# Kernel tuning notes

Hardware: AMD Instinct MI355X
Metric: run time of the kernel (lower is better)

The kernel has to match this reference:

```python
import jax, jax.numpy as jnp
import numpy as np

N = 20000
E = 600000
D = 512
H = 8
HD = D // H
HID = 1024
FIN = D + 3 * H  # forces_mlp input dim = 536
SCALE = 1.0 / float(np.sqrt(HD))


def _ln(x, g, b, eps=1e-5):
    m = x.mean(-1, keepdims=True)
    v = x.var(-1, keepdims=True)
    return (x - m) / jnp.sqrt(v + eps) * g + b


def _resmlp(h, Wi, bi, Wh, bh, Wo, bo):
    # ResMLP with layers=3: in-proj, one residual hidden block, out-proj
    h = jax.nn.gelu(h @ Wi + bi)
    h = h + jax.nn.gelu(h @ Wh + bh)
    return h @ Wo + bo


def setup_inputs() -> dict:
    key = jax.random.key(0)
    ks = jax.random.split(key, 24)
    s = 0.02
    x = jax.random.normal(ks[0], (N, D), jnp.float32)
    edge_index = jax.random.randint(ks[1], (2, E), 0, N, dtype=jnp.int32)
    att_bias = jax.random.normal(ks[2], (E,), jnp.float32)
    pos = jax.random.normal(ks[3], (N, 3), jnp.float32)
    batch = jnp.zeros((N,), jnp.int32)
    return {
        "x": x, "edge_index": edge_index, "att_bias": att_bias, "pos": pos, "batch": batch,
        "g_att": jnp.ones((D,), jnp.float32), "b_att": jnp.zeros((D,), jnp.float32),
        "g_mlp": jnp.ones((D,), jnp.float32), "b_mlp": jnp.zeros((D,), jnp.float32),
        "Wq": jax.random.normal(ks[4], (D, D), jnp.float32) * s, "bq": jnp.zeros((D,), jnp.float32),
        "Wk": jax.random.normal(ks[5], (D, D), jnp.float32) * s, "bk": jnp.zeros((D,), jnp.float32),
        "We_in": jax.random.normal(ks[6], (D, HID), jnp.float32) * s, "be_in": jnp.zeros((HID,), jnp.float32),
        "We_h": jax.random.normal(ks[7], (HID, HID), jnp.float32) * s, "be_h": jnp.zeros((HID,), jnp.float32),
        "We_out": jax.random.normal(ks[8], (HID, 1), jnp.float32) * s, "be_out": jnp.zeros((1,), jnp.float32),
        "Wf_in": jax.random.normal(ks[9], (FIN, HID), jnp.float32) * s, "bf_in": jnp.zeros((HID,), jnp.float32),
        "Wf_h": jax.random.normal(ks[10], (HID, HID), jnp.float32) * s, "bf_h": jnp.zeros((HID,), jnp.float32),
        "Wf_out": jax.random.normal(ks[11], (HID, 3), jnp.float32) * s, "bf_out": jnp.zeros((3,), jnp.float32),
    }


def reference(x, edge_index, att_bias, pos, batch,
              g_att, b_att, g_mlp, b_mlp, Wq, bq, Wk, bk,
              We_in, be_in, We_h, be_h, We_out, be_out,
              Wf_in, bf_in, Wf_h, bf_h, Wf_out, bf_out):
    n = x.shape[0]
    row, col = edge_index[0], edge_index[1]

    z_att = _ln(x, g_att, b_att)
    q = (z_att @ Wq + bq).reshape(n, H, HD)  # [N,H,HD]
    k = (z_att @ Wk + bk).reshape(n, H, HD)

    # sparse scaled dot product restricted to edges, with additive per-edge bias
    logits = jnp.einsum('ehd,ehd->eh', q[row], k[col]) * SCALE + att_bias[:, None]  # [E,H]
    mx = jax.ops.segment_max(logits, row, num_segments=n)          # [N,H]
    mx = jnp.where(jnp.isfinite(mx), mx, 0.0)
    p = jnp.exp(logits - mx[row])
    denom = jax.ops.segment_sum(p, row, num_segments=n)            # [N,H]
    w = p / denom[row]                                             # [E,H]

    contrib = jnp.einsum('eh,ec->ehc', w, pos[col])                # [E,H,3]
    att = jax.ops.segment_sum(contrib, row, num_segments=n)        # [N,H,3]
    att = att - pos[:, None, :]                                    # att - value
    att = att.reshape(n, H * 3)                                    # permute(1,0,2).view(N,-1)

    z_mlp = _ln(x, g_mlp, b_mlp)
    energy = _resmlp(z_mlp, We_in, be_in, We_h, be_h, We_out, be_out)
    forces = _resmlp(jnp.concatenate([z_mlp, att], axis=-1), Wf_in, bf_in, Wf_h, bf_h, Wf_out, bf_out)
    return (energy, forces)
```

## Files before the change

kernel.cpp:

```cpp
#include <hip/hip_runtime.h>
#include <hip/hip_fp16.h>

#define NN 20000
#define EE 600000

typedef unsigned short u16;
typedef unsigned char u8;
typedef unsigned int u32;
typedef float f32x4 __attribute__((ext_vector_type(4)));
typedef u32 u32x4 __attribute__((ext_vector_type(4)));
typedef u32 u32x2 __attribute__((ext_vector_type(2)));

__device__ __forceinline__ u16 f2bf(float f){
  u32 u = __float_as_uint(f);
  return (u16)((u + 0x7fffu + ((u>>16)&1u))>>16);
}
__device__ __forceinline__ float bf2f(u16 h){ return __uint_as_float(((u32)h)<<16); }

__device__ __forceinline__ u8 f2bf8(float v){
  __half h = __float2half(v);
  u16 b = *(u16*)&h;
  return (u8)((b + 0x7Fu + ((b>>8)&1u)) >> 8);
}
__device__ __forceinline__ float bf82f(u32 byte){
  __half_raw r; r.x = (u16)(byte << 8);
  return __half2float(__half(r));
}

__device__ __forceinline__ float gelu_f(float x){
  float u = 0.7978845608028654f*(x + 0.044715f*x*x*x);
  float e = __expf(2.0f*u);
  return 0.5f*x*(2.0f - 2.0f/(e+1.0f));
}

struct WttDesc { const float* W; u16* WT; int K, Nn, Kpad; };
struct WttPack { WttDesc d[6]; };

#define B_WTT  1536
#define B_PREP 313
#define B_LN2  5000
#define B_HIST 2344

__global__ __launch_bounds__(256) void misc_kernel(
    WttPack p,
    float* __restrict__ out, const float* __restrict__ beO, const float* __restrict__ bfO,
    float* __restrict__ bqk, const float* __restrict__ bq, const float* __restrict__ bk,
    float* __restrict__ bcat, const float* __restrict__ beI, const float* __restrict__ bfI,
    const float* __restrict__ x,
    const float* __restrict__ ga, const float* __restrict__ ba,
    const float* __restrict__ gm, const float* __restrict__ bm,
    u16* __restrict__ za, u16* __restrict__ xf,
    const int* __restrict__ ei, int* __restrict__ deg)
{
  __shared__ u16 tile[64][65];
  const int b = blockIdx.x;
  const int tid = threadIdx.x;
  if(b < B_WTT){
    const WttDesc dd = p.d[b >> 8];
    const int r8 = b & 255;
    const int k0 = (r8 & 15) << 6, n0 = (r8 >> 4) << 6;
    if(k0 >= dd.Kpad || n0 >= dd.Nn) return;
    const int tx = tid & 63, ty = tid >> 6;
#pragma unroll
    for(int i=0;i<16;i++){
      int r = (i<<2) + ty;
      int gk = k0 + r;
      float v = (gk < dd.K) ? dd.W[(size_t)gk*dd.Nn + n0 + tx] : 0.f;
      tile[r][tx] = f2bf(v);
    }
    __syncthreads();
#pragma unroll
    for(int i=0;i<16;i++){
      int r = (i<<2) + ty;
      dd.WT[(size_t)(n0 + r)*dd.Kpad + k0 + tx] = tile[tx][r];
    }
  } else if(b < B_WTT + B_PREP){
    int idx = (b - B_WTT)*256 + tid;
    if(idx < NN) out[idx] = beO[0];
    else if(idx < NN*4) out[idx] = bfO[(idx - NN) % 3];
    if(idx < 512) bqk[idx] = bq[idx];
    else if(idx < 1024) bqk[idx] = bk[idx-512];
    if(idx < 1024) bcat[idx] = beI[idx];
    else if(idx < 2048) bcat[idx] = bfI[idx-1024];
  } else if(b < B_WTT + B_PREP + B_LN2){
    int row = ((b - B_WTT - B_PREP)<<2) + (tid>>6);
    int lane = tid & 63;
    if(row >= NN) return;
    const float* xp = x + ((size_t)row<<9) + (lane<<3);
    f32x4 v0 = *(const f32x4*)xp;
    f32x4 v1 = *(const f32x4*)(xp+4);
    float vals[8] = {v0[0],v0[1],v0[2],v0[3],v1[0],v1[1],v1[2],v1[3]};
    float s=0.f, qs=0.f;
#pragma unroll
    for(int i=0;i<8;i++){ s += vals[i]; qs = fmaf(vals[i],vals[i],qs); }
#pragma unroll
    for(int o=1;o<64;o<<=1){ s += __shfl_xor(s,o); qs += __shfl_xor(qs,o); }
    float mean = s*(1.f/512.f);
    float var  = qs*(1.f/512.f) - mean*mean;
    float rstd = rsqrtf(var + 1e-5f);
    int c0 = lane<<3;
#pragma unroll
    for(int i=0;i<8;i++){
      float zn = (vals[i]-mean)*rstd;
      za[((size_t)row<<9)+c0+i] = f2bf(fmaf(zn, ga[c0+i], ba[c0+i]));
      xf[(size_t)row*576+c0+i]  = f2bf(fmaf(zn, gm[c0+i], bm[c0+i]));
    }
  } else {
    int e = (b - B_WTT - B_PREP - B_LN2)*256 + tid;
    if(e < EE) atomicAdd(&deg[ei[e]], 1);
  }
}

__global__ __launch_bounds__(256) void gemm_bt(
    const u16* __restrict__ A, const u16* __restrict__ B,
    const float* __restrict__ bias, const u16* __restrict__ resid,
    u16* __restrict__ Cb, u8* __restrict__ k8,
    const float* __restrict__ wout, float* __restrict__ outp,
    const u16* __restrict__ B2, const float* __restrict__ bias2,
    const float* __restrict__ wout2, float* __restrict__ outp2,
    int M, int N, int K, int lda, int ldr, int mode)
{
  __shared__ u16 As[128*64];
  __shared__ u16 Bs[128*64];
  const int gx = gridDim.x;
  const int b  = blockIdx.y*gx + blockIdx.x;
  const int xcd = b & 7, loc = b >> 3;
  int tileM, tileN, half = 0;
  const u16* Ab = A; const u16* Bp = B; const float* bp = bias;
  if(mode < 2){
    tileM = ((loc/gx)*8 + xcd) << 7;
    tileN = (loc % gx) << 7;
  } else {
    half = xcd >> 2;
    const int mt = ((loc>>3)<<2) + (xcd & 3);
    tileM = mt << 7;
    tileN = (loc & 7) << 7;
    if(half){ Ab = A + 1024; Bp = B2; bp = bias2; }
  }
  if(tileM >= M) return;
  const int tid  = threadIdx.x;
  const int wave = tid>>6, lane = tid&63;
  const int quad = lane>>4, l15 = lane&15;
  const int mhalf = (wave>>1)<<6, nhalf = (wave&1)<<6;
  f32x4 acc[4][4] = {};

  for(int k0=0; k0<K; k0+=64){
#pragma unroll
    for(int j=0;j<4;j++){
      const int c   = (((wave<<2)+j)<<6) + lane;
      const int row = c>>3;
      const int cc  = (c&7) ^ (row&7);
      int gr = tileM + row; gr = (gr < M) ? gr : (M-1);
      const u16* gp = Ab + (size_t)gr*lda + (size_t)(k0 + (cc<<3));
      __builtin_amdgcn_global_load_lds(
        (const __attribute__((address_space(1))) u32*)gp,
        (__attribute__((address_space(3))) u32*)(&As[((wave<<2)+j)<<9]),
        16, 0, 0);
    }
#pragma unroll
    for(int j=0;j<4;j++){
      const int c   = (((wave<<2)+j)<<6) + lane;
      const int row = c>>3;
      const int cc  = (c&7) ^ (row&7);
      const u16* gp = Bp + (size_t)(tileN + row)*K + (size_t)(k0 + (cc<<3));
      __builtin_amdgcn_global_load_lds(
        (const __attribute__((address_space(1))) u32*)gp,
        (__attribute__((address_space(3))) u32*)(&Bs[((wave<<2)+j)<<9]),
        16, 0, 0);
    }
    __syncthreads();
#pragma unroll
    for(int ks=0;ks<2;ks++){
      const int ccol = (ks<<2) + quad;
      u32x4 af[4], bfr[4];
#pragma unroll
      for(int mi=0;mi<4;mi++){
        const int row = mhalf + (mi<<4) + l15;
        af[mi] = *(const u32x4*)&As[((row<<3) + (ccol ^ (row&7)))<<3];
      }
#pragma unroll
      for(int ni=0;ni<4;ni++){
        const int row = nhalf + (ni<<4) + l15;
        bfr[ni] = *(const u32x4*)&Bs[((row<<3) + (ccol ^ (row&7)))<<3];
      }
#pragma unroll
      for(int mi=0;mi<4;mi++)
#pragma unroll
        for(int ni=0;ni<4;ni++)
          asm("v_mfma_f32_16x16x32_bf16 %0, %1, %2, %0"
              : "+v"(acc[mi][ni]) : "v"(af[mi]), "v"(bfr[ni]));
    }
    __syncthreads();
  }

  if(mode == 0){
#pragma unroll
    for(int mi=0;mi<4;mi++){
#pragma unroll
      for(int reg=0;reg<4;reg++){
        const int gr = tileM + mhalf + (mi<<4) + (quad<<2) + reg;
        if(gr < M){
#pragma unroll
          for(int ni=0;ni<4;ni++){
            const int gc = tileN + nhalf + (ni<<4) + l15;
            float v = acc[mi][ni][reg] + bp[gc];
            if(gc < 512) Cb[(size_t)gr*512 + gc] = f2bf(v);
            else         k8[(size_t)gr*512 + gc - 512] = f2bf8(v);
          }
        }
      }
    }
  } else if(mode == 1){
#pragma unroll
    for(int mi=0;mi<4;mi++){
#pragma unroll
      for(int reg=0;reg<4;reg++){
        const int gr = tileM + mhalf + (mi<<4) + (quad<<2) + reg;
        if(gr < M){
#pragma unroll
          for(int ni=0;ni<4;ni++){
            const int gc = tileN + nhalf + (ni<<4) + l15;
            Cb[(size_t)gr*N + gc] = f2bf(gelu_f(acc[mi][ni][reg] + bp[gc]));
          }
        }
      }
    }
  } else if(!half){
    float wv[4], bv[4];
#pragma unroll
    for(int ni=0;ni<4;ni++){
      int gc = tileN + nhalf + (ni<<4) + l15;
      wv[ni] = wout[gc]; bv[ni] = bp[gc];
    }
#pragma unroll
    for(int mi=0;mi<4;mi++){
#pragma unroll
      for(int reg=0;reg<4;reg++){
        const int gr = tileM + mhalf + (mi<<4) + (quad<<2) + reg;
        if(gr < M){
          float vs = 0.f;
#pragma unroll
          for(int ni=0;ni<4;ni++){
            const int gc = tileN + nhalf + (ni<<4) + l15;
            float v = gelu_f(acc[mi][ni][reg] + bv[ni])
                    + bf2f(resid[(size_t)gr*ldr + gc]);
            vs = fmaf(v, wv[ni], vs);
          }
          vs += __shfl_xor(vs,1); vs += __shfl_xor(vs,2);
          vs += __shfl_xor(vs,4); vs += __shfl_xor(vs,8);
          if(l15 == 0) atomicAdd(&outp[gr], vs);
        }
      }
    }
  } else {
    float wv0[4], wv1[4], wv2[4], bv[4];
#pragma unroll
    for(int ni=0;ni<4;ni++){
      int gc = tileN + nhalf + (ni<<4) + l15;
      wv0[ni] = wout2[gc*3+0]; wv1[ni] = wout2[gc*3+1]; wv2[ni] = wout2[gc*3+2];
      bv[ni] = bp[gc];
    }
#pragma unroll
    for(int mi=0;mi<4;mi++){
#pragma unroll
      for(int reg=0;reg<4;reg++){
        const int gr = tileM + mhalf + (mi<<4) + (quad<<2) + reg;
        if(gr < M){
          float s0=0.f, s1=0.f, s2=0.f;
#pragma unroll
          for(int ni=0;ni<4;ni++){
            const int gc = tileN + nhalf + (ni<<4) + l15;
            float v = gelu_f(acc[mi][ni][reg] + bv[ni])
                    + bf2f(resid[(size_t)gr*ldr + 1024 + gc]);
            s0 = fmaf(v, wv0[ni], s0);
            s1 = fmaf(v, wv1[ni], s1);
            s2 = fmaf(v, wv2[ni], s2);
          }
          s0 += __shfl_xor(s0,1); s0 += __shfl_xor(s0,2); s0 += __shfl_xor(s0,4); s0 += __shfl_xor(s0,8);
          s1 += __shfl_xor(s1,1); s1 += __shfl_xor(s1,2); s1 += __shfl_xor(s1,4); s1 += __shfl_xor(s1,8);
          s2 += __shfl_xor(s2,1); s2 += __shfl_xor(s2,2); s2 += __shfl_xor(s2,4); s2 += __shfl_xor(s2,8);
          if(l15 == 0){
            atomicAdd(&outp2[(size_t)gr*3+0], s0);
            atomicAdd(&outp2[(size_t)gr*3+1], s1);
            atomicAdd(&outp2[(size_t)gr*3+2], s2);
          }
        }
      }
    }
  }
}

__global__ __launch_bounds__(1024) void scan_kernel(
    const int* __restrict__ deg, int* __restrict__ rowptr,
    int* __restrict__ cursor, int N)
{
  __shared__ int wsum[16];
  __shared__ int carry_s;
  const int tid = threadIdx.x, lane = tid & 63, wid = tid >> 6;
  if(tid == 0) carry_s = 0;
  __syncthreads();
  for(int base = 0; base < N; base += 1024){
    int idx = base + tid;
    int v = (idx < N) ? deg[idx] : 0;
    int s = v;
#pragma unroll
    for(int o=1;o<64;o<<=1){ int t = __shfl_up(s,o); if(lane>=o) s += t; }
    if(lane==63) wsum[wid] = s;
    __syncthreads();
    if(wid==0 && lane<16){
      int ws = wsum[lane];
      int t = ws;
#pragma unroll
      for(int o=1;o<16;o<<=1){ int u = __shfl_up(t,o); if(lane>=o) t += u; }
      wsum[lane] = t - ws;
    }
    __syncthreads();
    int ex = s - v + wsum[wid] + carry_s;
    if(idx < N){ rowptr[idx] = ex; cursor[idx] = ex; }
    __syncthreads();
    if(tid == 1023) carry_s += wsum[15] + s;
  }
  __syncthreads();
  if(tid == 0) rowptr[N] = carry_s;
}

__global__ __launch_bounds__(256) void scatter_kernel(
    const int* __restrict__ ei, const float* __restrict__ ab,
    int* __restrict__ cursor, int* __restrict__ cols,
    float* __restrict__ abs_, int E)
{
  int e = blockIdx.x*256 + threadIdx.x;
  if(e >= E) return;
  int r = ei[e];
  int p = atomicAdd(&cursor[r], 1);
  cols[p] = ei[EE + e];
  abs_[p] = ab[e];
}

__global__ __launch_bounds__(256) void node_att_kernel(
    const u16* __restrict__ qd, const u8* __restrict__ k8,
    const int* __restrict__ rowptr, const int* __restrict__ cols,
    const float* __restrict__ abs_, const float* __restrict__ pos,
    u16* __restrict__ xf, int N)
{
  const int node = (blockIdx.x<<2) + (threadIdx.x>>6);
  const int lane = threadIdx.x & 63;
  if(node >= N) return;
  const int h = lane>>3, sub = lane&7;
  const u32x4 qv = *(const u32x4*)(qd + ((size_t)node<<9) + (lane<<3));
  float qf[8];
#pragma unroll
  for(int i=0;i<4;i++){
    qf[2*i]   = __uint_as_float(qv[i]<<16);
    qf[2*i+1] = __uint_as_float(qv[i]&0xffff0000u);
  }
  const float posn = (sub<3) ? pos[node*3 + sub] : 0.f;
  const int j1 = rowptr[node+1];
  float den = 0.f, nm = 0.f;

  int j = rowptr[node];
  for(; j+7 < j1; j += 8){
    int c[8]; float abv[8], pv[8]; u32x2 kw[8];
#pragma unroll
    for(int t=0;t<8;t++){ c[t] = cols[j+t]; abv[t] = abs_[j+t]; }
#pragma unroll
    for(int t=0;t<8;t++){
      kw[t] = *(const u32x2*)(k8 + ((size_t)c[t]<<9) + (lane<<3));
      pv[t] = (sub<3) ? pos[c[t]*3+sub] : 0.f;
    }
#pragma unroll
    for(int t=0;t<8;t++){
      float s = 0.f;
#pragma unroll
      for(int i=0;i<8;i++){
        u32 byte = (kw[t][i>>2] >> ((i&3)<<3)) & 0xFFu;
        s = fmaf(qf[i], bf82f(byte), s);
      }
      s += __shfl_xor(s,1); s += __shfl_xor(s,2); s += __shfl_xor(s,4);
      float p = __expf(fmaf(s, 0.125f, abv[t]));
      den += p;
      nm = fmaf(p, pv[t], nm);
    }
  }
  for(; j < j1; j++){
    int c0 = cols[j];
    u32x2 kw0 = *(const u32x2*)(k8 + ((size_t)c0<<9) + (lane<<3));
    float pv0 = (sub<3) ? pos[c0*3+sub] : 0.f;
    float s0=0.f;
#pragma unroll
    for(int i=0;i<8;i++){
      u32 byte = (kw0[i>>2] >> ((i&3)<<3)) & 0xFFu;
      s0 = fmaf(qf[i], bf82f(byte), s0);
    }
    s0 += __shfl_xor(s0,1); s0 += __shfl_xor(s0,2); s0 += __shfl_xor(s0,4);
    float p0 = __expf(fmaf(s0, 0.125f, abs_[j]));
    den += p0;
    nm = fmaf(p0, pv0, nm);
  }

  u16* xp = xf + (size_t)node*576;
  if(sub < 3){
    float a = (den > 0.f) ? nm/den : 0.f;
    xp[512 + h*3 + sub] = f2bf(a - posn);
  } else {
    xp[536 + h*5 + (sub-3)] = 0;
  }
}

extern "C" void kernel_launch(void* const* d_in, const int* in_sizes, int n_in,
                              void* d_out, int out_size, void* d_ws, size_t ws_size,
                              hipStream_t stream)
{
  (void)in_sizes; (void)n_in; (void)out_size; (void)ws_size;
  const float* x    = (const float*)d_in[0];
  const int*   ei   = (const int*)d_in[1];
  const float* ab   = (const float*)d_in[2];
  const float* pos  = (const float*)d_in[3];
  const float* g_att= (const float*)d_in[5];
  const float* b_att= (const float*)d_in[6];
  const float* g_mlp= (const float*)d_in[7];
  const float* b_mlp= (const float*)d_in[8];
  const float* Wq   = (const float*)d_in[9];  const float* bq  = (const float*)d_in[10];
  const float* Wk   = (const float*)d_in[11]; const float* bk  = (const float*)d_in[12];
  const float* WeI  = (const float*)d_in[13]; const float* beI = (const float*)d_in[14];
  const float* WeH  = (const float*)d_in[15]; const float* beH = (const float*)d_in[16];
  const float* WeO  = (const float*)d_in[17]; const float* beO = (const float*)d_in[18];
  const float* WfI  = (const float*)d_in[19]; const float* bfI = (const float*)d_in[20];
  const float* WfH  = (const float*)d_in[21]; const float* bfH = (const float*)d_in[22];
  const float* WfO  = (const float*)d_in[23]; const float* bfO = (const float*)d_in[24];

  char* w = (char*)d_ws;
  size_t off = 0;
  auto alloc = [&](size_t bytes) -> void* {
    void* p = w + off; off += (bytes + 255) & ~(size_t)255; return p;
  };
  u16* zatt  = (u16*)alloc((size_t)NN*512*2);
  u16* qd    = (u16*)alloc((size_t)NN*512*2);
  u8*  k8    = (u8*) alloc((size_t)NN*512);
  u16* xf    = (u16*)alloc((size_t)NN*576*2);
  u16* h1cat = (u16*)alloc((size_t)NN*2048*2);
  u16* wqkT  = (u16*)alloc((size_t)1024*512*2);
  u16* wInT  = (u16*)alloc((size_t)2048*576*2);
  u16* weHT  = (u16*)alloc((size_t)1024*1024*2);
  u16* wfHT  = (u16*)alloc((size_t)1024*1024*2);
  float* bqk    = (float*)alloc((size_t)1024*4);
  float* bcat   = (float*)alloc((size_t)2048*4);
  int*   deg    = (int*)alloc((size_t)NN*4);
  int*   rowptr = (int*)alloc((size_t)(NN+1)*4);
  int*   cursor = (int*)alloc((size_t)NN*4);
  int*   cols   = (int*)alloc((size_t)EE*4);
  float* absrt  = (float*)alloc((size_t)EE*4);

  hipMemsetAsync(deg, 0, (size_t)NN*4, stream);

  WttPack pk;
  pk.d[0] = { Wq,  wqkT,            512,  512,  512 };
  pk.d[1] = { Wk,  wqkT + 512*512,  512,  512,  512 };
  pk.d[2] = { WeI, wInT,            512,  1024, 576 };
  pk.d[3] = { WfI, wInT + 1024*576, 536,  1024, 576 };
  pk.d[4] = { WeH, weHT,            1024, 1024, 1024 };
  pk.d[5] = { WfH, wfHT,            1024, 1024, 1024 };
  misc_kernel<<<dim3(B_WTT+B_PREP+B_LN2+B_HIST),256,0,stream>>>(
      pk, (float*)d_out, beO, bfO, bqk, bq, bk, bcat, beI, bfI,
      x, g_att, b_att, g_mlp, b_mlp, zatt, xf, ei, deg);

  scan_kernel   <<<1,1024,0,stream>>>(deg, rowptr, cursor, NN);
  scatter_kernel<<<dim3((EE+255)/256),256,0,stream>>>(ei, ab, cursor, cols, absrt, EE);

  const int MT = 160;

  gemm_bt<<<dim3(8, MT),256,0,stream>>>(zatt, wqkT, bqk, nullptr, qd, k8,
                                        nullptr, nullptr,
                                        nullptr, nullptr, nullptr, nullptr,
                                        NN, 1024, 512, 512, 0, 0);

  node_att_kernel<<<dim3((NN+3)/4),256,0,stream>>>(qd, k8, rowptr, cols, absrt, pos, xf, NN);

  gemm_bt<<<dim3(16, MT),256,0,stream>>>(xf, wInT, bcat, nullptr, h1cat, nullptr,
                                         nullptr, nullptr,
                                         nullptr, nullptr, nullptr, nullptr,
                                         NN, 2048, 576, 576, 0, 1);

  gemm_bt<<<dim3(8, 2*MT),256,0,stream>>>(h1cat, weHT, beH, h1cat, nullptr, nullptr,
                                          WeO, (float*)d_out,
                                          wfHT, bfH, WfO, (float*)d_out + NN,
                                          NN, 1024, 1024, 2048, 2048, 2);
}
```

Measured before the change: 513.6 us.

## Co-schedule independent GEMMs with scatter and attention via merged launch kernels

Splits the fused input-projection GEMM into an energy part (K=512, reading only the LN columns of xf) and a forces part (K=576). The energy GEMM runs in the same launch as the edge attention, and the QK GEMM runs in the same launch as the CSR scatter, so independent work overlaps instead of running in sequence. This is meant to cut launch gaps and tail idle time and to drop the concatenated bias buffer. The trade-off is one extra GEMM launch, mixed block types within a grid, and more weight transpose work for the split layout.

```diff
diff --git a/kernel.cpp b/kernel.cpp
--- a/kernel.cpp
+++ b/kernel.cpp
@@ -45,7 +45,6 @@
     WttPack p,
     float* __restrict__ out, const float* __restrict__ beO, const float* __restrict__ bfO,
     float* __restrict__ bqk, const float* __restrict__ bq, const float* __restrict__ bk,
-    float* __restrict__ bcat, const float* __restrict__ beI, const float* __restrict__ bfI,
     const float* __restrict__ x,
     const float* __restrict__ ga, const float* __restrict__ ba,
     const float* __restrict__ gm, const float* __restrict__ bm,
@@ -80,8 +79,6 @@
     else if(idx < NN*4) out[idx] = bfO[(idx - NN) % 3];
     if(idx < 512) bqk[idx] = bq[idx];
     else if(idx < 1024) bqk[idx] = bk[idx-512];
-    if(idx < 1024) bcat[idx] = beI[idx];
-    else if(idx < 2048) bcat[idx] = bfI[idx-1024];
   } else if(b < B_WTT + B_PREP + B_LN2){
     int row = ((b - B_WTT - B_PREP)<<2) + (tid>>6);
     int lane = tid & 63;
@@ -111,32 +108,219 @@
   }
 }
 
-__global__ __launch_bounds__(256) void gemm_bt(
+struct GemmP {
+  const u16* A; const u16* B; const float* bias;
+  u16* Cb; u8* k8; int M, K, lda, ldc, mode;
+};
+
+__device__ __forceinline__ void gemm01(const GemmP g, int vb)
+{
+  __shared__ u16 As[128*64];
+  __shared__ u16 Bs[128*64];
+  const int xcd = vb & 7, loc = vb >> 3;
+  const int tileM = (((loc>>3)<<3) + xcd) << 7;
+  const int tileN = (loc & 7) << 7;
+  if(tileM >= g.M) return;
+  const int tid  = threadIdx.x;
+  const int wave = tid>>6, lane = tid&63;
+  const int quad = lane>>4, l15 = lane&15;
+  const int mhalf = (wave>>1)<<6, nhalf = (wave&1)<<6;
+  f32x4 acc[4][4] = {};
+
+  for(int k0=0; k0<g.K; k0+=64){
+#pragma unroll
+    for(int j=0;j<4;j++){
+      const int c   = (((wave<<2)+j)<<6) + lane;
+      const int row = c>>3;
+      const int cc  = (c&7) ^ (row&7);
+      int gr = tileM + row; gr = (gr < g.M) ? gr : (g.M-1);
+      const u16* gp = g.A + (size_t)gr*g.lda + (size_t)(k0 + (cc<<3));
+      __builtin_amdgcn_global_load_lds(
+        (const __attribute__((address_space(1))) u32*)gp,
+        (__attribute__((address_space(3))) u32*)(&As[((wave<<2)+j)<<9]),
+        16, 0, 0);
+    }
+#pragma unroll
+    for(int j=0;j<4;j++){
+      const int c   = (((wave<<2)+j)<<6) + lane;
+      const int row = c>>3;
+      const int cc  = (c&7) ^ (row&7);
+      const u16* gp = g.B + (size_t)(tileN + row)*g.K + (size_t)(k0 + (cc<<3));
+      __builtin_amdgcn_global_load_lds(
+        (const __attribute__((address_space(1))) u32*)gp,
+        (__attribute__((address_space(3))) u32*)(&Bs[((wave<<2)+j)<<9]),
+        16, 0, 0);
+    }
+    __syncthreads();
+#pragma unroll
+    for(int ks=0;ks<2;ks++){
+      const int ccol = (ks<<2) + quad;
+      u32x4 af[4], bfr[4];
+#pragma unroll
+      for(int mi=0;mi<4;mi++){
+        const int row = mhalf + (mi<<4) + l15;
+        af[mi] = *(const u32x4*)&As[((row<<3) + (ccol ^ (row&7)))<<3];
+      }
+#pragma unroll
+      for(int ni=0;ni<4;ni++){
+        const int row = nhalf + (ni<<4) + l15;
+        bfr[ni] = *(const u32x4*)&Bs[((row<<3) + (ccol ^ (row&7)))<<3];
+      }
+#pragma unroll
+      for(int mi=0;mi<4;mi++)
+#pragma unroll
+        for(int ni=0;ni<4;ni++)
+          asm("v_mfma_f32_16x16x32_bf16 %0, %1, %2, %0"
+              : "+v"(acc[mi][ni]) : "v"(af[mi]), "v"(bfr[ni]));
+    }
+    __syncthreads();
+  }
+
+#pragma unroll
+  for(int mi=0;mi<4;mi++){
+#pragma unroll
+    for(int reg=0;reg<4;reg++){
+      const int gr = tileM + mhalf + (mi<<4) + (quad<<2) + reg;
+      if(gr < g.M){
+#pragma unroll
+        for(int ni=0;ni<4;ni++){
+          const int gc = tileN + nhalf + (ni<<4) + l15;
+          float v = acc[mi][ni][reg] + g.bias[gc];
+          if(g.mode == 0){
+            if(gc < 512) g.Cb[(size_t)gr*512 + gc] = f2bf(v);
+            else         g.k8[(size_t)gr*512 + gc - 512] = f2bf8(v);
+          } else {
+            g.Cb[(size_t)gr*g.ldc + gc] = f2bf(gelu_f(v));
+          }
+        }
+      }
+    }
+  }
+}
+
+__device__ __forceinline__ void node_att_body(
+    int vb, const u16* __restrict__ qd, const u8* __restrict__ k8,
+    const int* __restrict__ rowptr, const int* __restrict__ cols,
+    const float* __restrict__ abs_, const float* __restrict__ pos,
+    u16* __restrict__ xf)
+{
+  const int node = (vb<<2) + (threadIdx.x>>6);
+  const int lane = threadIdx.x & 63;
+  if(node >= NN) return;
+  const int h = lane>>3, sub = lane&7;
+  const u32x4 qv = *(const u32x4*)(qd + ((size_t)node<<9) + (lane<<3));
+  float qf[8];
+#pragma unroll
+  for(int i=0;i<4;i++){
+    qf[2*i]   = __uint_as_float(qv[i]<<16);
+    qf[2*i+1] = __uint_as_float(qv[i]&0xffff0000u);
+  }
+  const float posn = (sub<3) ? pos[node*3 + sub] : 0.f;
+  const int j1 = rowptr[node+1];
+  float den = 0.f, nm = 0.f;
+
+  int j = rowptr[node];
+  for(; j+7 < j1; j += 8){
+    int c[8]; float abv[8], pv[8]; u32x2 kw[8];
+#pragma unroll
+    for(int t=0;t<8;t++){ c[t] = cols[j+t]; abv[t] = abs_[j+t]; }
+#pragma unroll
+    for(int t=0;t<8;t++){
+      kw[t] = *(const u32x2*)(k8 + ((size_t)c[t]<<9) + (lane<<3));
+      pv[t] = (sub<3) ? pos[c[t]*3+sub] : 0.f;
+    }
+#pragma unroll
+    for(int t=0;t<8;t++){
+      float s = 0.f;
+#pragma unroll
+      for(int i=0;i<8;i++){
+        u32 byte = (kw[t][i>>2] >> ((i&3)<<3)) & 0xFFu;
+        s = fmaf(qf[i], bf82f(byte), s);
+      }
+      s += __shfl_xor(s,1); s += __shfl_xor(s,2); s += __shfl_xor(s,4);
+      float p = __expf(fmaf(s, 0.125f, abv[t]));
+      den += p;
+      nm = fmaf(p, pv[t], nm);
+    }
+  }
+  for(; j < j1; j++){
+    int c0 = cols[j];
+    u32x2 kw0 = *(const u32x2*)(k8 + ((size_t)c0<<9) + (lane<<3));
+    float pv0 = (sub<3) ? pos[c0*3+sub] : 0.f;
+    float s0=0.f;
+#pragma unroll
+    for(int i=0;i<8;i++){
+      u32 byte = (kw0[i>>2] >> ((i&3)<<3)) & 0xFFu;
+      s0 = fmaf(qf[i], bf82f(byte), s0);
+    }
+    s0 += __shfl_xor(s0,1); s0 += __shfl_xor(s0,2); s0 += __shfl_xor(s0,4);
+    float p0 = __expf(fmaf(s0, 0.125f, abs_[j]));
+    den += p0;
+    nm = fmaf(p0, pv0, nm);
+  }
+
+  u16* xp = xf + (size_t)node*576;
+  if(sub < 3){
+    float a = (den > 0.f) ? nm/den : 0.f;
+    xp[512 + h*3 + sub] = f2bf(a - posn);
+  } else {
+    xp[536 + h*5 + (sub-3)] = 0;
+  }
+}
+
+__global__ __launch_bounds__(256) void mega1_kernel(
+    GemmP g, const int* __restrict__ ei, const float* __restrict__ ab,
+    int* __restrict__ cursor, int* __restrict__ cols, float* __restrict__ abs_)
+{
+  const int b = blockIdx.x;
+  if(b < 1280){
+    gemm01(g, b);
+  } else {
+    int e = (b - 1280)*256 + threadIdx.x;
+    if(e >= EE) return;
+    int r = ei[e];
+    int p = atomicAdd(&cursor[r], 1);
+    cols[p] = ei[EE + e];
+    abs_[p] = ab[e];
+  }
+}
+
+__global__ __launch_bounds__(256) void mega2_kernel(
+    GemmP g, const u16* __restrict__ qd, const u8* __restrict__ k8,
+    const int* __restrict__ rowptr, const int* __restrict__ cols,
+    const float* __restrict__ abs_, const float* __restrict__ pos,
+    u16* __restrict__ xf)
+{
+  const int b = blockIdx.x;
+  if(b < 1280) gemm01(g, b);
+  else         node_att_body(b - 1280, qd, k8, rowptr, cols, abs_, pos, xf);
+}
+
+__global__ __launch_bounds__(256) void gemm01_kernel(GemmP g)
+{
+  gemm01(g, blockIdx.x);
+}
+
+__global__ __launch_bounds__(256) void gemm_hidden(
     const u16* __restrict__ A, const u16* __restrict__ B,
     const float* __restrict__ bias, const u16* __restrict__ resid,
-    u16* __restrict__ Cb, u8* __restrict__ k8,
     const float* __restrict__ wout, float* __restrict__ outp,
     const u16* __restrict__ B2, const float* __restrict__ bias2,
     const float* __restrict__ wout2, float* __restrict__ outp2,
-    int M, int N, int K, int lda, int ldr, int mode)
+    int M, int K, int lda, int ldr)
 {
   __shared__ u16 As[128*64];
   __shared__ u16 Bs[128*64];
   const int gx = gridDim.x;
   const int b  = blockIdx.y*gx + blockIdx.x;
   const int xcd = b & 7, loc = b >> 3;
-  int tileM, tileN, half = 0;
-  const u16* Ab = A; const u16* Bp = B; const float* bp = bias;
-  if(mode < 2){
-    tileM = ((loc/gx)*8 + xcd) << 7;
-    tileN = (loc % gx) << 7;
-  } else {
-    half = xcd >> 2;
-    const int mt = ((loc>>3)<<2) + (xcd & 3);
-    tileM = mt << 7;
-    tileN = (loc & 7) << 7;
-    if(half){ Ab = A + 1024; Bp = B2; bp = bias2; }
-  }
+  const int half = xcd >> 2;
+  const int mt = ((loc>>3)<<2) + (xcd & 3);
+  const int tileM = mt << 7;
+  const int tileN = (loc & 7) << 7;
+  const u16* Ab = half ? (A + 1024) : A;
+  const u16* Bp = half ? B2 : B;
+  const float* bp = half ? bias2 : bias;
   if(tileM >= M) return;
   const int tid  = threadIdx.x;
   const int wave = tid>>6, lane = tid&63;
@@ -193,39 +377,7 @@
     __syncthreads();
   }
 
-  if(mode == 0){
-#pragma unroll
-    for(int mi=0;mi<4;mi++){
-#pragma unroll
-      for(int reg=0;reg<4;reg++){
-        const int gr = tileM + mhalf + (mi<<4) + (quad<<2) + reg;
-        if(gr < M){
-#pragma unroll
-          for(int ni=0;ni<4;ni++){
-            const int gc = tileN + nhalf + (ni<<4) + l15;
-            float v = acc[mi][ni][reg] + bp[gc];
-            if(gc < 512) Cb[(size_t)gr*512 + gc] = f2bf(v);
-            else         k8[(size_t)gr*512 + gc - 512] = f2bf8(v);
-          }
-        }
-      }
-    }
-  } else if(mode == 1){
-#pragma unroll
-    for(int mi=0;mi<4;mi++){
-#pragma unroll
-      for(int reg=0;reg<4;reg++){
-        const int gr = tileM + mhalf + (mi<<4) + (quad<<2) + reg;
-        if(gr < M){
-#pragma unroll
-          for(int ni=0;ni<4;ni++){
-            const int gc = tileN + nhalf + (ni<<4) + l15;
-            Cb[(size_t)gr*N + gc] = f2bf(gelu_f(acc[mi][ni][reg] + bp[gc]));
-          }
-        }
-      }
-    }
-  } else if(!half){
+  if(!half){
     float wv[4], bv[4];
 #pragma unroll
     for(int ni=0;ni<4;ni++){
@@ -324,89 +476,6 @@
   if(tid == 0) rowptr[N] = carry_s;
 }
 
-__global__ __launch_bounds__(256) void scatter_kernel(
-    const int* __restrict__ ei, const float* __restrict__ ab,
-    int* __restrict__ cursor, int* __restrict__ cols,
-    float* __restrict__ abs_, int E)
-{
-  int e = blockIdx.x*256 + threadIdx.x;
-  if(e >= E) return;
-  int r = ei[e];
-  int p = atomicAdd(&cursor[r], 1);
-  cols[p] = ei[EE + e];
-  abs_[p] = ab[e];
-}
-
-__global__ __launch_bounds__(256) void node_att_kernel(
-    const u16* __restrict__ qd, const u8* __restrict__ k8,
-    const int* __restrict__ rowptr, const int* __restrict__ cols,
-    const float* __restrict__ abs_, const float* __restrict__ pos,
-    u16* __restrict__ xf, int N)
-{
-  const int node = (blockIdx.x<<2) + (threadIdx.x>>6);
-  const int lane = threadIdx.x & 63;
-  if(node >= N) return;
-  const int h = lane>>3, sub = lane&7;
-  const u32x4 qv = *(const u32x4*)(qd + ((size_t)node<<9) + (lane<<3));
-  float qf[8];
-#pragma unroll
-  for(int i=0;i<4;i++){
-    qf[2*i]   = __uint_as_float(qv[i]<<16);
-    qf[2*i+1] = __uint_as_float(qv[i]&0xffff0000u);
-  }
-  const float posn = (sub<3) ? pos[node*3 + sub] : 0.f;
-  const int j1 = rowptr[node+1];
-  float den = 0.f, nm = 0.f;
-
-  int j = rowptr[node];
-  for(; j+7 < j1; j += 8){
-    int c[8]; float abv[8], pv[8]; u32x2 kw[8];
-#pragma unroll
-    for(int t=0;t<8;t++){ c[t] = cols[j+t]; abv[t] = abs_[j+t]; }
-#pragma unroll
-    for(int t=0;t<8;t++){
-      kw[t] = *(const u32x2*)(k8 + ((size_t)c[t]<<9) + (lane<<3));
-      pv[t] = (sub<3) ? pos[c[t]*3+sub] : 0.f;
-    }
-#pragma unroll
-    for(int t=0;t<8;t++){
-      float s = 0.f;
-#pragma unroll
-      for(int i=0;i<8;i++){
-        u32 byte = (kw[t][i>>2] >> ((i&3)<<3)) & 0xFFu;
-        s = fmaf(qf[i], bf82f(byte), s);
-      }
-      s += __shfl_xor(s,1); s += __shfl_xor(s,2); s += __shfl_xor(s,4);
-      float p = __expf(fmaf(s, 0.125f, abv[t]));
-      den += p;
-      nm = fmaf(p, pv[t], nm);
-    }
-  }
-  for(; j < j1; j++){
-    int c0 = cols[j];
-    u32x2 kw0 = *(const u32x2*)(k8 + ((size_t)c0<<9) + (lane<<3));
-    float pv0 = (sub<3) ? pos[c0*3+sub] : 0.f;
-    float s0=0.f;
-#pragma unroll
-    for(int i=0;i<8;i++){
-      u32 byte = (kw0[i>>2] >> ((i&3)<<3)) & 0xFFu;
-      s0 = fmaf(qf[i], bf82f(byte), s0);
-    }
-    s0 += __shfl_xor(s0,1); s0 += __shfl_xor(s0,2); s0 += __shfl_xor(s0,4);
-    float p0 = __expf(fmaf(s0, 0.125f, abs_[j]));
-    den += p0;
-    nm = fmaf(p0, pv0, nm);
-  }
-
-  u16* xp = xf + (size_t)node*576;
-  if(sub < 3){
-    float a = (den > 0.f) ? nm/den : 0.f;
-    xp[512 + h*3 + sub] = f2bf(a - posn);
-  } else {
-    xp[536 + h*5 + (sub-3)] = 0;
-  }
-}
-
 extern "C" void kernel_launch(void* const* d_in, const int* in_sizes, int n_in,
                               void* d_out, int out_size, void* d_ws, size_t ws_size,
                               hipStream_t stream)
@@ -440,11 +509,11 @@
   u16* xf    = (u16*)alloc((size_t)NN*576*2);
   u16* h1cat = (u16*)alloc((size_t)NN*2048*2);
   u16* wqkT  = (u16*)alloc((size_t)1024*512*2);
-  u16* wInT  = (u16*)alloc((size_t)2048*576*2);
+  u16* weIT  = (u16*)alloc((size_t)1024*512*2);
+  u16* wfIT  = (u16*)alloc((size_t)1024*576*2);
   u16* weHT  = (u16*)alloc((size_t)1024*1024*2);
   u16* wfHT  = (u16*)alloc((size_t)1024*1024*2);
   float* bqk    = (float*)alloc((size_t)1024*4);
-  float* bcat   = (float*)alloc((size_t)2048*4);
   int*   deg    = (int*)alloc((size_t)NN*4);
   int*   rowptr = (int*)alloc((size_t)(NN+1)*4);
   int*   cursor = (int*)alloc((size_t)NN*4);
@@ -454,35 +523,29 @@
   hipMemsetAsync(deg, 0, (size_t)NN*4, stream);
 
   WttPack pk;
-  pk.d[0] = { Wq,  wqkT,            512,  512,  512 };
-  pk.d[1] = { Wk,  wqkT + 512*512,  512,  512,  512 };
-  pk.d[2] = { WeI, wInT,            512,  1024, 576 };
-  pk.d[3] = { WfI, wInT + 1024*576, 536,  1024, 576 };
-  pk.d[4] = { WeH, weHT,            1024, 1024, 1024 };
-  pk.d[5] = { WfH, wfHT,            1024, 1024, 1024 };
+  pk.d[0] = { Wq,  wqkT, 512,  512,  512 };
+  pk.d[1] = { Wk,  wqkT + 512*512, 512, 512, 512 };
+  pk.d[2] = { WeI, weIT, 512,  1024, 512 };
+  pk.d[3] = { WfI, wfIT, 536,  1024, 576 };
+  pk.d[4] = { WeH, weHT, 1024, 1024, 1024 };
+  pk.d[5] = { WfH, wfHT, 1024, 1024, 1024 };
   misc_kernel<<<dim3(B_WTT+B_PREP+B_LN2+B_HIST),256,0,stream>>>(
-      pk, (float*)d_out, beO, bfO, bqk, bq, bk, bcat, beI, bfI,
+      pk, (float*)d_out, beO, bfO, bqk, bq, bk,
       x, g_att, b_att, g_mlp, b_mlp, zatt, xf, ei, deg);
 
-  scan_kernel   <<<1,1024,0,stream>>>(deg, rowptr, cursor, NN);
-  scatter_kernel<<<dim3((EE+255)/256),256,0,stream>>>(ei, ab, cursor, cols, absrt, EE);
-
-  const int MT = 160;
-
-  gemm_bt<<<dim3(8, MT),256,0,stream>>>(zatt, wqkT, bqk, nullptr, qd, k8,
-                                        nullptr, nullptr,
-                                        nullptr, nullptr, nullptr, nullptr,
-                                        NN, 1024, 512, 512, 0, 0);
-
-  node_att_kernel<<<dim3((NN+3)/4),256,0,stream>>>(qd, k8, rowptr, cols, absrt, pos, xf, NN);
-
-  gemm_bt<<<dim3(16, MT),256,0,stream>>>(xf, wInT, bcat, nullptr, h1cat, nullptr,
-                                         nullptr, nullptr,
-                                         nullptr, nullptr, nullptr, nullptr,
-                                         NN, 2048, 576, 576, 0, 1);
-
-  gemm_bt<<<dim3(8, 2*MT),256,0,stream>>>(h1cat, weHT, beH, h1cat, nullptr, nullptr,
-                                          WeO, (float*)d_out,
-                                          wfHT, bfH, WfO, (float*)d_out + NN,
-                                          NN, 1024, 1024, 2048, 2048, 2);
-}
+  scan_kernel<<<1,1024,0,stream>>>(deg, rowptr, cursor, NN);
+
+  GemmP gqk = { zatt, wqkT, bqk, qd, k8, NN, 512, 512, 512, 0 };
+  mega1_kernel<<<dim3(1280 + 2344),256,0,stream>>>(gqk, ei, ab, cursor, cols, absrt);
+
+  GemmP gie = { xf, weIT, beI, h1cat, nullptr, NN, 512, 576, 2048, 1 };
+  mega2_kernel<<<dim3(1280 + 5000),256,0,stream>>>(gie, qd, k8, rowptr, cols, absrt, pos, xf);
+
+  GemmP gif = { xf, wfIT, bfI, h1cat + 1024, nullptr, NN, 576, 576, 2048, 1 };
+  gemm01_kernel<<<dim3(1280),256,0,stream>>>(gif);
+
+  gemm_hidden<<<dim3(8, 320),256,0,stream>>>(h1cat, weHT, beH, h1cat,
+                                             WeO, (float*)d_out,
+                                             wfHT, bfH, WfO, (float*)d_out + NN,
+                                             NN, 1024, 2048, 2048);
+}
```

New measurement: 569.5 us. 10.9% more time.
